# Kernel optimization log

Hardware: AMD Instinct MI355X
Metric: run time of the kernel (lower is better)

Reference implementation:

```python
import jax, jax.numpy as jnp
import numpy as np

B, T, D_MODEL, N_HEADS = 2, 2048, 1024, 16


def setup_inputs() -> dict:
    key = jax.random.key(0)
    ks = jax.random.split(key, 5)
    w_scale = 0.02
    return {
        "x": jax.random.normal(ks[0], (B, T, D_MODEL), jnp.float32),
        "Wq": jax.random.normal(ks[1], (D_MODEL, D_MODEL), jnp.float32) * w_scale,
        "Wk": jax.random.normal(ks[2], (D_MODEL, D_MODEL), jnp.float32) * w_scale,
        "Wv": jax.random.normal(ks[3], (D_MODEL, D_MODEL), jnp.float32) * w_scale,
        "Wo": jax.random.normal(ks[4], (D_MODEL, D_MODEL), jnp.float32) * w_scale,
    }


def reference(x, Wq, Wk, Wv, Wo):
    Bv, Tv, _ = x.shape
    H = N_HEADS
    D = D_MODEL // H
    # Projections (torch nn.Linear: y = x @ W.T), split heads -> (B, H, T, D)
    q = (x @ Wq.T).reshape(Bv, Tv, H, D).transpose(0, 2, 1, 3)
    k = (x @ Wk.T).reshape(Bv, Tv, H, D).transpose(0, 2, 1, 3)
    v = (x @ Wv.T).reshape(Bv, Tv, H, D).transpose(0, 2, 1, 3)

    scale = jnp.sqrt(jnp.asarray(D, jnp.float32))
    scores = jnp.einsum("bhqd,bhkd->bhqk", q, k) / scale  # (B, H, T, T)

    # ALiBi bias: -|i-j| * slope_h, future positions masked to -inf (causal)
    slopes = jnp.asarray(
        [2.0 ** (-8.0 * h / H) for h in range(1, H + 1)], jnp.float32
    )
    pos = jnp.arange(Tv)
    dist = jnp.abs(pos[None, :] - pos[:, None]).astype(jnp.float32)  # (T, T)
    bias = -dist[None, :, :] * slopes[:, None, None]                 # (H, T, T)
    causal_mask = jnp.triu(jnp.ones((Tv, Tv), dtype=bool), 1)
    bias = jnp.where(causal_mask[None, :, :], -jnp.inf, bias)
    scores = scores + bias[None]  # (B, H, T, T)

    attn = jax.nn.softmax(scores, axis=-1)
    out = jnp.einsum("bhqk,bhkd->bhqd", attn, v)
    out = out.transpose(0, 2, 1, 3).reshape(Bv, Tv, D_MODEL)
    return out @ Wo.T
```

## Files before the change

### kernel.cpp

```cpp
#include <hip/hip_runtime.h>


#define DEV __device__ __forceinline__

typedef __attribute__((ext_vector_type(8))) short short8;
typedef __attribute__((ext_vector_type(4))) float f32x4;
typedef __attribute__((ext_vector_type(4))) unsigned short ushort4v;

DEV unsigned short f2bf(float f) {
  unsigned u = __builtin_bit_cast(unsigned, f);
  u += 0x7fffu + ((u >> 16) & 1u);
  return (unsigned short)(u >> 16);
}
DEV float bf2f(unsigned short u) {
  unsigned x = ((unsigned)u) << 16;
  return __builtin_bit_cast(float, x);
}

DEV void gl2lds16(const void* g, void* l) {
  __builtin_amdgcn_global_load_lds(
      (const __attribute__((address_space(1))) void*)g,
      (__attribute__((address_space(3))) void*)l, 16, 0, 0);
}

__global__ __launch_bounds__(256) void cvt_all(
    const float* __restrict__ x, const float* __restrict__ wq,
    const float* __restrict__ wk, const float* __restrict__ wv,
    const float* __restrict__ wo, unsigned short* __restrict__ xb,
    unsigned short* __restrict__ wqb, unsigned short* __restrict__ wkb,
    unsigned short* __restrict__ wvb, unsigned short* __restrict__ wob) {
  int b = blockIdx.x;
  const float* s;
  unsigned short* d;
  int off;
  if (b < 4096)      { s = x;  d = xb;  off = b; }
  else if (b < 5120) { s = wq; d = wqb; off = b - 4096; }
  else if (b < 6144) { s = wk; d = wkb; off = b - 5120; }
  else if (b < 7168) { s = wv; d = wvb; off = b - 6144; }
  else               { s = wo; d = wob; off = b - 7168; }
  int i = (off * 256 + threadIdx.x) * 4;
  float4 v = *(const float4*)(s + i);
  ushort4v o = {f2bf(v.x), f2bf(v.y), f2bf(v.z), f2bf(v.w)};
  *(ushort4v*)(d + i) = o;
}

__global__ __launch_bounds__(256, 2) void gemm_qkv(
    const unsigned short* __restrict__ A, const unsigned short* __restrict__ Wq,
    const unsigned short* __restrict__ Wk, const unsigned short* __restrict__ Wv,
    unsigned short* __restrict__ Qo, unsigned short* __restrict__ Ko,
    unsigned short* __restrict__ Vo) {
  constexpr int K = 1024;
  __shared__ alignas(16) unsigned short Sm[18432];
  unsigned short* Al = Sm;
  unsigned short* Bl = Sm + 4096;
  const int t = threadIdx.x;
  const int l = t & 63, l15 = l & 15, l4 = l >> 4;
  const int wm = ((t >> 6) & 1) * 64, wn = (t >> 7) * 64;
  const int wsel = blockIdx.x >> 3;
  const int n0 = (blockIdx.x & 7) * 128;
  const int m0 = blockIdx.y * 128;
  const unsigned short* Bm = (wsel == 0) ? Wq : ((wsel == 1) ? Wk : Wv);

  f32x4 zero4 = {0.f, 0.f, 0.f, 0.f};
  f32x4 acc[4][4];
#pragma unroll
  for (int i = 0; i < 4; i++)
#pragma unroll
    for (int j = 0; j < 4; j++) acc[i][j] = zero4;

  const int row0 = t >> 2, seg = (t & 3) * 8;
  const unsigned short* Ag0 = A + (m0 + row0) * K + seg;
  const unsigned short* Ag1 = A + (m0 + row0 + 64) * K + seg;
  const unsigned short* Bg0 = Bm + (n0 + row0) * K + seg;
  const unsigned short* Bg1 = Bm + (n0 + row0 + 64) * K + seg;

  for (int k0 = 0; k0 < K; k0 += 32) {
    gl2lds16(Ag0 + k0, &Al[t * 8]);
    gl2lds16(Ag1 + k0, &Al[2048 + t * 8]);
    gl2lds16(Bg0 + k0, &Bl[t * 8]);
    gl2lds16(Bg1 + k0, &Bl[2048 + t * 8]);
    __syncthreads();
    short8 af[4], bf8[4];
#pragma unroll
    for (int mi = 0; mi < 4; mi++)
      af[mi] = *(const short8*)&Al[(wm + mi * 16 + l15) * 32 + l4 * 8];
#pragma unroll
    for (int ni = 0; ni < 4; ni++)
      bf8[ni] = *(const short8*)&Bl[(wn + ni * 16 + l15) * 32 + l4 * 8];
#pragma unroll
    for (int mi = 0; mi < 4; mi++)
#pragma unroll
      for (int ni = 0; ni < 4; ni++)
        acc[mi][ni] = __builtin_amdgcn_mfma_f32_16x16x32_bf16(
            af[mi], bf8[ni], acc[mi][ni], 0, 0, 0);
    __syncthreads();
  }

  if (wsel != 2) {
    unsigned short* D = (wsel == 0) ? Qo : Ko;
    const float scale = (wsel == 0) ? 0.18033688011112042f : 1.0f;
#pragma unroll
    for (int mi = 0; mi < 4; mi++)
#pragma unroll
      for (int r = 0; r < 4; r++) {
        int m = m0 + wm + mi * 16 + l4 * 4 + r;
        int b = m >> 11, tt = m & 2047;
#pragma unroll
        for (int ni = 0; ni < 4; ni++) {
          int n = n0 + wn + ni * 16 + l15;
          int z = b * 16 + (n >> 6), d = n & 63;
          D[(z * 2048 + tt) * 64 + d] = f2bf(acc[mi][ni][r] * scale);
        }
      }
  } else {
    unsigned short* Tr = Sm + (t >> 6) * 4608;
#pragma unroll
    for (int mi = 0; mi < 4; mi++)
#pragma unroll
      for (int r = 0; r < 4; r++) {
        int tl = mi * 16 + l4 * 4 + r;
#pragma unroll
        for (int ni = 0; ni < 4; ni++)
          Tr[(ni * 16 + l15) * 72 + tl] = f2bf(acc[mi][ni][r]);
      }
    __syncthreads();
    const int bb = m0 >> 11, tbase = m0 & 2047;
#pragma unroll
    for (int it2 = 0; it2 < 8; it2++) {
      int idx = it2 * 256 + t;
      int row = idx >> 4, c = idx & 15;
      int zh = row >> 6, dd = row & 63;
      int wsrc = zh * 2 + (c >> 3);
      short8 v = *(const short8*)&Sm[wsrc * 4608 + dd * 72 + (c & 7) * 8];
      int zg = bb * 16 + (n0 >> 6) + zh;
      *(short8*)&Vo[(zg * 64 + dd) * 2048 + tbase + c * 8] = v;
    }
  }
}

__global__ __launch_bounds__(256, 2) void gemm_o(
    const unsigned short* __restrict__ A, const unsigned short* __restrict__ Bm,
    float* __restrict__ C) {
  constexpr int K = 1024;
  __shared__ alignas(16) unsigned short Al[128 * 32];
  __shared__ alignas(16) unsigned short Bl[64 * 32];
  const int t = threadIdx.x;
  const int l = t & 63, l15 = l & 15, l4 = l >> 4;
  const int wm = ((t >> 6) & 1) * 64, wn = (t >> 7) * 32;
  const int m0 = blockIdx.y * 128, n0 = blockIdx.x * 64;

  f32x4 zero4 = {0.f, 0.f, 0.f, 0.f};
  f32x4 acc[4][2];
#pragma unroll
  for (int i = 0; i < 4; i++)
#pragma unroll
    for (int j = 0; j < 2; j++) acc[i][j] = zero4;

  const int row0 = t >> 2, seg = (t & 3) * 8;
  const unsigned short* Ag0 = A + (m0 + row0) * K + seg;
  const unsigned short* Ag1 = A + (m0 + row0 + 64) * K + seg;
  const unsigned short* Bg0 = Bm + (n0 + row0) * K + seg;

  for (int k0 = 0; k0 < K; k0 += 32) {
    gl2lds16(Ag0 + k0, &Al[t * 8]);
    gl2lds16(Ag1 + k0, &Al[2048 + t * 8]);
    gl2lds16(Bg0 + k0, &Bl[t * 8]);
    __syncthreads();
    short8 af[4], bf2[2];
#pragma unroll
    for (int mi = 0; mi < 4; mi++)
      af[mi] = *(const short8*)&Al[(wm + mi * 16 + l15) * 32 + l4 * 8];
#pragma unroll
    for (int ni = 0; ni < 2; ni++)
      bf2[ni] = *(const short8*)&Bl[(wn + ni * 16 + l15) * 32 + l4 * 8];
#pragma unroll
    for (int mi = 0; mi < 4; mi++)
#pragma unroll
      for (int ni = 0; ni < 2; ni++)
        acc[mi][ni] = __builtin_amdgcn_mfma_f32_16x16x32_bf16(
            af[mi], bf2[ni], acc[mi][ni], 0, 0, 0);
    __syncthreads();
  }
#pragma unroll
  for (int mi = 0; mi < 4; mi++)
#pragma unroll
    for (int r = 0; r < 4; r++) {
      int m = m0 + wm + mi * 16 + l4 * 4 + r;
      float* cp = C + m * 1024 + n0 + wn + l15;
      cp[0] = acc[mi][0][r];
      cp[16] = acc[mi][1][r];
    }
}

__global__ __launch_bounds__(256, 3) void flash_alibi(
    const unsigned short* __restrict__ Q, const unsigned short* __restrict__ Kb,
    const unsigned short* __restrict__ Vt, unsigned short* __restrict__ O0,
    unsigned short* __restrict__ O1, float* __restrict__ L0,
    float* __restrict__ L1) {
  __shared__ alignas(16) unsigned short Kl[2 * 4096];
  __shared__ alignas(16) unsigned short Vl[2 * 4096];
  __shared__ alignas(16) unsigned short Pl[4 * 2304];
  const int t = threadIdx.x, w = t >> 6, l = t & 63, l15 = l & 15, l4 = l >> 4;
  const int g = blockIdx.x;
  const int qt = 15 - (g >> 6);
  const int z = (g & 63) >> 1, s = g & 1;
  const int q0 = qt * 128, h = z & 15;
  const float slope2 = exp2f(-0.5f * (float)(h + 1)) * 1.4426950408889634f;
  const int qrow = q0 + w * 32;

  short8 aq[2][2];
#pragma unroll
  for (int mi = 0; mi < 2; mi++)
#pragma unroll
    for (int ks = 0; ks < 2; ks++)
      aq[mi][ks] = *(const short8*)&Q[(z * 2048 + qrow + mi * 16 + l15) * 64 +
                                      ks * 32 + l4 * 8];

  f32x4 binit[2];
#pragma unroll
  for (int mi = 0; mi < 2; mi++)
#pragma unroll
    for (int r = 0; r < 4; r++)
      binit[mi][r] = -(slope2 * (float)(qrow + mi * 16 + l4 * 4 + r) + 10.0f);

  f32x4 zero4 = {0.f, 0.f, 0.f, 0.f};
  f32x4 o[2][4];
  float lsum[2][4];
#pragma unroll
  for (int mi = 0; mi < 2; mi++)
#pragma unroll
    for (int j = 0; j < 4; j++) {
      o[mi][j] = zero4;
      lsum[mi][j] = 0.f;
    }

  const int row0 = t >> 2, seg8 = (t & 3) * 8;
  const int it0 = s ? (qt + 1) : 0;
  const int nt = qt + 1;

#define ISSUE_LOADS(KV0, BUF)                                                \
  {                                                                          \
    unsigned short* Kd = &Kl[(BUF) * 4096];                                  \
    unsigned short* Vd = &Vl[(BUF) * 4096];                                  \
    gl2lds16(&Kb[(z * 2048 + (KV0) + row0) * 64 + seg8], &Kd[t * 8]);        \
    gl2lds16(&Kb[(z * 2048 + (KV0) + row0) * 64 + 32 + seg8],                \
             &Kd[2048 + t * 8]);                                             \
    gl2lds16(&Vt[(z * 64 + row0) * 2048 + (KV0) + seg8], &Vd[t * 8]);        \
    gl2lds16(&Vt[(z * 64 + row0) * 2048 + (KV0) + 32 + seg8],                \
             &Vd[2048 + t * 8]);                                             \
  }

  ISSUE_LOADS(it0 * 64, 0)

  for (int ii = 0; ii < nt; ++ii) {
    __syncthreads();
    const int kv0 = (it0 + ii) * 64;
    if (ii + 1 < nt) ISSUE_LOADS(kv0 + 64, (ii + 1) & 1)
    if (kv0 > qrow + 31) continue;
    const unsigned short* Kc = &Kl[(ii & 1) * 4096];
    const unsigned short* Vc = &Vl[(ii & 1) * 4096];

    f32x4 sc[2][4];
#pragma unroll
    for (int mi = 0; mi < 2; mi++)
#pragma unroll
      for (int ni = 0; ni < 4; ni++) sc[mi][ni] = binit[mi];
#pragma unroll
    for (int ks = 0; ks < 2; ks++) {
      short8 bk[4];
#pragma unroll
      for (int ni = 0; ni < 4; ni++)
        bk[ni] = *(const short8*)&Kc[(ks * 64 + ni * 16 + l15) * 32 + l4 * 8];
#pragma unroll
      for (int mi = 0; mi < 2; mi++)
#pragma unroll
        for (int ni = 0; ni < 4; ni++)
          sc[mi][ni] = __builtin_amdgcn_mfma_f32_16x16x32_bf16(
              aq[mi][ks], bk[ni], sc[mi][ni], 0, 0, 0);
    }

    const bool needMask = (kv0 + 63 > qrow);
    float jf[4];
#pragma unroll
    for (int ni = 0; ni < 4; ni++) jf[ni] = (float)(kv0 + ni * 16 + l15);

#pragma unroll
    for (int mi = 0; mi < 2; mi++)
#pragma unroll
      for (int r = 0; r < 4; r++) {
        float ps[4];
#pragma unroll
        for (int ni = 0; ni < 4; ni++)
          ps[ni] = __builtin_amdgcn_exp2f(fmaf(slope2, jf[ni], sc[mi][ni][r]));
        if (needMask) {
          int qi = qrow + mi * 16 + l4 * 4 + r;
#pragma unroll
          for (int ni = 0; ni < 4; ni++)
            if (kv0 + ni * 16 + l15 > qi) ps[ni] = 0.f;
        }
        lsum[mi][r] += (ps[0] + ps[1]) + (ps[2] + ps[3]);
        int row = mi * 16 + l4 * 4 + r;
        unsigned short* pp = &Pl[w * 2304 + row * 72 + (l15 & 7)];
#pragma unroll
        for (int ni = 0; ni < 4; ni++)
          pp[((ni * 2 + (l15 >> 3)) ^ l4) * 8] = f2bf(ps[ni]);
      }

    asm volatile("s_waitcnt lgkmcnt(0)" ::: "memory");

    const int rsw = (l15 >> 2) & 3;
#pragma unroll
    for (int ks = 0; ks < 2; ks++) {
      short8 pf[2], vf[4];
#pragma unroll
      for (int mi = 0; mi < 2; mi++)
        pf[mi] = *(const short8*)&Pl[w * 2304 + (mi * 16 + l15) * 72 +
                                     ((ks * 4 + l4) ^ rsw) * 8];
#pragma unroll
      for (int nd = 0; nd < 4; nd++)
        vf[nd] = *(const short8*)&Vc[(ks * 64 + nd * 16 + l15) * 32 + l4 * 8];
#pragma unroll
      for (int mi = 0; mi < 2; mi++)
#pragma unroll
        for (int nd = 0; nd < 4; nd++)
          o[mi][nd] = __builtin_amdgcn_mfma_f32_16x16x32_bf16(
              pf[mi], vf[nd], o[mi][nd], 0, 0, 0);
    }
  }
#undef ISSUE_LOADS

  unsigned short* Op = s ? O1 : O0;
  float* Lp = s ? L1 : L0;
#pragma unroll
  for (int mi = 0; mi < 2; mi++)
#pragma unroll
    for (int r = 0; r < 4; r++) {
      float lv = lsum[mi][r];
#pragma unroll
      for (int off = 1; off < 16; off <<= 1) lv += __shfl_xor(lv, off);
      int tg = qrow + mi * 16 + l4 * 4 + r;
      if (l15 == 0) Lp[z * 2048 + tg] = lv;
      unsigned short* op = &Op[(z * 2048 + tg) * 64 + l15];
#pragma unroll
      for (int nd = 0; nd < 4; nd++) op[nd * 16] = f2bf(o[mi][nd][r]);
    }
}

__global__ __launch_bounds__(256) void combine(
    const unsigned short* __restrict__ O0, const unsigned short* __restrict__ O1,
    const float* __restrict__ L0, const float* __restrict__ L1,
    unsigned short* __restrict__ Ob) {
  int idx = (blockIdx.x * 256 + threadIdx.x) * 8;
  int z = idx >> 17, rem = idx & 131071;
  int tt = rem >> 6, d = rem & 63;
  short8 a = *(const short8*)(O0 + idx);
  short8 b = *(const short8*)(O1 + idx);
  float inv = 1.0f / (L0[z * 2048 + tt] + L1[z * 2048 + tt]);
  short8 o;
#pragma unroll
  for (int j = 0; j < 8; j++) {
    float v = (bf2f((unsigned short)a[j]) + bf2f((unsigned short)b[j])) * inv;
    o[j] = (short)f2bf(v);
  }
  int bq = z >> 4, h = z & 15;
  *(short8*)(Ob + (bq * 2048 + tt) * 1024 + h * 64 + d) = o;
}

extern "C" void kernel_launch(void* const* d_in, const int* in_sizes, int n_in,
                              void* d_out, int out_size, void* d_ws,
                              size_t ws_size, hipStream_t stream) {
  const float* x = (const float*)d_in[0];
  const float* Wq = (const float*)d_in[1];
  const float* Wk = (const float*)d_in[2];
  const float* Wv = (const float*)d_in[3];
  const float* Wo = (const float*)d_in[4];

  char* p = (char*)d_ws;
  unsigned short* xb = (unsigned short*)p;  p += 4096 * 1024 * 2;
  unsigned short* wqb = (unsigned short*)p; p += 1024 * 1024 * 2;
  unsigned short* wkb = (unsigned short*)p; p += 1024 * 1024 * 2;
  unsigned short* wvb = (unsigned short*)p; p += 1024 * 1024 * 2;
  unsigned short* wob = (unsigned short*)p; p += 1024 * 1024 * 2;
  unsigned short* Qb = (unsigned short*)p;  p += 32 * 2048 * 64 * 2;
  unsigned short* Kbf = (unsigned short*)p; p += 32 * 2048 * 64 * 2;
  unsigned short* Vtb = (unsigned short*)p; p += 32 * 2048 * 64 * 2;
  unsigned short* O1 = (unsigned short*)p;  p += 32 * 2048 * 64 * 2;
  float* L0 = (float*)p;                    p += 32 * 2048 * 4;
  float* L1 = (float*)p;                    p += 32 * 2048 * 4;
  unsigned short* O0 = xb;
  unsigned short* Ob = Qb;

  cvt_all<<<8192, 256, 0, stream>>>(x, Wq, Wk, Wv, Wo, xb, wqb, wkb, wvb, wob);
  gemm_qkv<<<dim3(24, 32), 256, 0, stream>>>(xb, wqb, wkb, wvb, Qb, Kbf, Vtb);
  flash_alibi<<<1024, 256, 0, stream>>>(Qb, Kbf, Vtb, O0, O1, L0, L1);
  combine<<<2048, 256, 0, stream>>>(O0, O1, L0, L1, Ob);
  gemm_o<<<dim3(16, 32), 256, 0, stream>>>(Ob, wob, (float*)d_out);
}
```

Before: 178.0 us.

## Compute transposed scores so P stays in registers, dropping the LDS round trip

The flash kernel now computes S^T (K as the A operand, Q as B) so each lane holds scores for one query row across consecutive keys. The probabilities are packed to bf16 and redistributed across lanes with xor shuffles to form the PV MFMA operand directly, which removes the per-warp P shared-memory buffer, its writes and reads, and the lgkmcnt wait. Freeing that LDS allows occupancy hints to be raised for both the flash and QKV GEMM kernels. In exchange it adds shuffle and select instructions per tile, and the higher occupancy targets may force register spills.

```diff
diff --git a/kernel.cpp b/kernel.cpp
--- a/kernel.cpp
+++ b/kernel.cpp
@@ -6,6 +6,7 @@
 typedef __attribute__((ext_vector_type(8))) short short8;
 typedef __attribute__((ext_vector_type(4))) float f32x4;
 typedef __attribute__((ext_vector_type(4))) unsigned short ushort4v;
+typedef __attribute__((ext_vector_type(4))) unsigned int uint4v;
 
 DEV unsigned short f2bf(float f) {
   unsigned u = __builtin_bit_cast(unsigned, f);
@@ -15,6 +16,9 @@
 DEV float bf2f(unsigned short u) {
   unsigned x = ((unsigned)u) << 16;
   return __builtin_bit_cast(float, x);
+}
+DEV unsigned packbf(float lo, float hi) {
+  return (unsigned)f2bf(lo) | ((unsigned)f2bf(hi) << 16);
 }
 
 DEV void gl2lds16(const void* g, void* l) {
@@ -44,7 +48,7 @@
   *(ushort4v*)(d + i) = o;
 }
 
-__global__ __launch_bounds__(256, 2) void gemm_qkv(
+__global__ __launch_bounds__(256, 3) void gemm_qkv(
     const unsigned short* __restrict__ A, const unsigned short* __restrict__ Wq,
     const unsigned short* __restrict__ Wk, const unsigned short* __restrict__ Wv,
     unsigned short* __restrict__ Qo, unsigned short* __restrict__ Ko,
@@ -192,14 +196,13 @@
     }
 }
 
-__global__ __launch_bounds__(256, 3) void flash_alibi(
+__global__ __launch_bounds__(256, 4) void flash_alibi(
     const unsigned short* __restrict__ Q, const unsigned short* __restrict__ Kb,
     const unsigned short* __restrict__ Vt, unsigned short* __restrict__ O0,
     unsigned short* __restrict__ O1, float* __restrict__ L0,
     float* __restrict__ L1) {
   __shared__ alignas(16) unsigned short Kl[2 * 4096];
   __shared__ alignas(16) unsigned short Vl[2 * 4096];
-  __shared__ alignas(16) unsigned short Pl[4 * 2304];
   const int t = threadIdx.x, w = t >> 6, l = t & 63, l15 = l & 15, l4 = l >> 4;
   const int g = blockIdx.x;
   const int qt = 15 - (g >> 6);
@@ -216,23 +219,17 @@
       aq[mi][ks] = *(const short8*)&Q[(z * 2048 + qrow + mi * 16 + l15) * 64 +
                                       ks * 32 + l4 * 8];
 
-  f32x4 binit[2];
-#pragma unroll
-  for (int mi = 0; mi < 2; mi++)
-#pragma unroll
-    for (int r = 0; r < 4; r++)
-      binit[mi][r] = -(slope2 * (float)(qrow + mi * 16 + l4 * 4 + r) + 10.0f);
+  const int qv0 = qrow + l15, qv1 = qrow + 16 + l15;
+  const float binit0 = -(slope2 * (float)qv0 + 10.0f);
+  const float binit1 = -(slope2 * (float)qv1 + 10.0f);
 
   f32x4 zero4 = {0.f, 0.f, 0.f, 0.f};
-  f32x4 o[2][4];
-  float lsum[2][4];
-#pragma unroll
-  for (int mi = 0; mi < 2; mi++)
-#pragma unroll
-    for (int j = 0; j < 4; j++) {
-      o[mi][j] = zero4;
-      lsum[mi][j] = 0.f;
-    }
+  f32x4 ot[4][2];
+  float lsum[2] = {0.f, 0.f};
+#pragma unroll
+  for (int nd = 0; nd < 4; nd++)
+#pragma unroll
+    for (int mi = 0; mi < 2; mi++) ot[nd][mi] = zero4;
 
   const int row0 = t >> 2, seg8 = (t & 3) * 8;
   const int it0 = s ? (qt + 1) : 0;
@@ -260,11 +257,14 @@
     const unsigned short* Kc = &Kl[(ii & 1) * 4096];
     const unsigned short* Vc = &Vl[(ii & 1) * 4096];
 
-    f32x4 sc[2][4];
-#pragma unroll
-    for (int mi = 0; mi < 2; mi++)
-#pragma unroll
-      for (int ni = 0; ni < 4; ni++) sc[mi][ni] = binit[mi];
+    f32x4 sc[4][2];
+#pragma unroll
+    for (int ni = 0; ni < 4; ni++) {
+      f32x4 b0 = {binit0, binit0, binit0, binit0};
+      f32x4 b1 = {binit1, binit1, binit1, binit1};
+      sc[ni][0] = b0;
+      sc[ni][1] = b1;
+    }
 #pragma unroll
     for (int ks = 0; ks < 2; ks++) {
       short8 bk[4];
@@ -272,59 +272,65 @@
       for (int ni = 0; ni < 4; ni++)
         bk[ni] = *(const short8*)&Kc[(ks * 64 + ni * 16 + l15) * 32 + l4 * 8];
 #pragma unroll
-      for (int mi = 0; mi < 2; mi++)
-#pragma unroll
-        for (int ni = 0; ni < 4; ni++)
-          sc[mi][ni] = __builtin_amdgcn_mfma_f32_16x16x32_bf16(
-              aq[mi][ks], bk[ni], sc[mi][ni], 0, 0, 0);
+      for (int ni = 0; ni < 4; ni++)
+#pragma unroll
+        for (int mi = 0; mi < 2; mi++)
+          sc[ni][mi] = __builtin_amdgcn_mfma_f32_16x16x32_bf16(
+              bk[ni], aq[mi][ks], sc[ni][mi], 0, 0, 0);
     }
 
     const bool needMask = (kv0 + 63 > qrow);
-    float jf[4];
-#pragma unroll
-    for (int ni = 0; ni < 4; ni++) jf[ni] = (float)(kv0 + ni * 16 + l15);
-
-#pragma unroll
-    for (int mi = 0; mi < 2; mi++)
-#pragma unroll
-      for (int r = 0; r < 4; r++) {
-        float ps[4];
-#pragma unroll
-        for (int ni = 0; ni < 4; ni++)
-          ps[ni] = __builtin_amdgcn_exp2f(fmaf(slope2, jf[ni], sc[mi][ni][r]));
-        if (needMask) {
-          int qi = qrow + mi * 16 + l4 * 4 + r;
-#pragma unroll
-          for (int ni = 0; ni < 4; ni++)
-            if (kv0 + ni * 16 + l15 > qi) ps[ni] = 0.f;
-        }
-        lsum[mi][r] += (ps[0] + ps[1]) + (ps[2] + ps[3]);
-        int row = mi * 16 + l4 * 4 + r;
-        unsigned short* pp = &Pl[w * 2304 + row * 72 + (l15 & 7)];
-#pragma unroll
-        for (int ni = 0; ni < 4; ni++)
-          pp[((ni * 2 + (l15 >> 3)) ^ l4) * 8] = f2bf(ps[ni]);
-      }
-
-    asm volatile("s_waitcnt lgkmcnt(0)" ::: "memory");
-
-    const int rsw = (l15 >> 2) & 3;
+
 #pragma unroll
     for (int ks = 0; ks < 2; ks++) {
-      short8 pf[2], vf[4];
-#pragma unroll
-      for (int mi = 0; mi < 2; mi++)
-        pf[mi] = *(const short8*)&Pl[w * 2304 + (mi * 16 + l15) * 72 +
-                                     ((ks * 4 + l4) ^ rsw) * 8];
+      short8 vf[4];
 #pragma unroll
       for (int nd = 0; nd < 4; nd++)
         vf[nd] = *(const short8*)&Vc[(ks * 64 + nd * 16 + l15) * 32 + l4 * 8];
-#pragma unroll
-      for (int mi = 0; mi < 2; mi++)
+
+      unsigned pk[2][2][2];
+#pragma unroll
+      for (int nip = 0; nip < 2; nip++) {
+        int ni = 2 * ks + nip;
+        int kvb = kv0 + ni * 16 + l4 * 4;
+#pragma unroll
+        for (int mi = 0; mi < 2; mi++) {
+          int qv = mi ? qv1 : qv0;
+          float p[4];
+#pragma unroll
+          for (int r = 0; r < 4; r++) {
+            p[r] = __builtin_amdgcn_exp2f(
+                fmaf(slope2, (float)(kvb + r), sc[ni][mi][r]));
+            if (needMask && (kvb + r > qv)) p[r] = 0.f;
+          }
+          lsum[mi] += (p[0] + p[1]) + (p[2] + p[3]);
+          pk[nip][mi][0] = packbf(p[0], p[1]);
+          pk[nip][mi][1] = packbf(p[2], p[3]);
+        }
+      }
+#pragma unroll
+      for (int mi = 0; mi < 2; mi++) {
+        unsigned wd[4];
+#pragma unroll
+        for (int sx = 0; sx < 2; sx++) {
+          unsigned X = pk[0][mi][sx], Y = pk[1][mi][sx];
+          unsigned M = (l4 < 2) ? X : Y;
+          unsigned N = (l4 < 2) ? Y : X;
+          unsigned Mx16 = __shfl_xor((int)M, 16);
+          unsigned Nx32 = __shfl_xor((int)N, 32);
+          unsigned Nx48 = __shfl_xor((int)N, 48);
+          wd[sx] = (l4 & 2) ? ((l4 & 1) ? Mx16 : Nx32)
+                            : ((l4 & 1) ? Nx48 : M);
+          wd[2 + sx] = (l4 & 2) ? ((l4 & 1) ? M : Nx48)
+                                : ((l4 & 1) ? Nx32 : Mx16);
+        }
+        uint4v uw = {wd[0], wd[1], wd[2], wd[3]};
+        short8 pf = __builtin_bit_cast(short8, uw);
 #pragma unroll
         for (int nd = 0; nd < 4; nd++)
-          o[mi][nd] = __builtin_amdgcn_mfma_f32_16x16x32_bf16(
-              pf[mi], vf[nd], o[mi][nd], 0, 0, 0);
+          ot[nd][mi] = __builtin_amdgcn_mfma_f32_16x16x32_bf16(
+              vf[nd], pf, ot[nd][mi], 0, 0, 0);
+      }
     }
   }
 #undef ISSUE_LOADS
@@ -332,18 +338,18 @@
   unsigned short* Op = s ? O1 : O0;
   float* Lp = s ? L1 : L0;
 #pragma unroll
-  for (int mi = 0; mi < 2; mi++)
-#pragma unroll
-    for (int r = 0; r < 4; r++) {
-      float lv = lsum[mi][r];
-#pragma unroll
-      for (int off = 1; off < 16; off <<= 1) lv += __shfl_xor(lv, off);
-      int tg = qrow + mi * 16 + l4 * 4 + r;
-      if (l15 == 0) Lp[z * 2048 + tg] = lv;
-      unsigned short* op = &Op[(z * 2048 + tg) * 64 + l15];
-#pragma unroll
-      for (int nd = 0; nd < 4; nd++) op[nd * 16] = f2bf(o[mi][nd][r]);
-    }
+  for (int mi = 0; mi < 2; mi++) {
+    float lv = lsum[mi];
+    lv += __shfl_xor(lv, 16);
+    lv += __shfl_xor(lv, 32);
+    int qg = qrow + mi * 16 + l15;
+    if (l4 == 0) Lp[z * 2048 + qg] = lv;
+    unsigned short* op = &Op[(z * 2048 + qg) * 64 + l4 * 4];
+#pragma unroll
+    for (int nd = 0; nd < 4; nd++)
+#pragma unroll
+      for (int r = 0; r < 4; r++) op[nd * 16 + r] = f2bf(ot[nd][mi][r]);
+  }
 }
 
 __global__ __launch_bounds__(256) void combine(
```

Measured after the change: 191.4 us. 7.5% more time.
